# Optimization experiments

Hardware: AMD Instinct MI355X
Metric: run time of the kernel (lower is better)

## Reference

```python
import jax, jax.numpy as jnp
import numpy as np

N_NODES = 50000
N_EDGES = 800000
D_IN = 128
D_HID = 256


def setup_inputs() -> dict:
    key = jax.random.key(0)
    ks = jax.random.split(key, 8)
    x = jax.random.normal(ks[0], (N_NODES, D_IN), dtype=jnp.float32)
    edge_index = jax.random.randint(ks[1], (2, N_EDGES), 0, N_NODES, dtype=jnp.int32)
    s1 = 1.0 / np.sqrt(D_IN)
    s2 = 1.0 / np.sqrt(D_HID)
    W1_l = jax.random.uniform(ks[2], (D_IN, D_HID), jnp.float32, -s1, s1)
    W1_r = jax.random.uniform(ks[3], (D_IN, D_HID), jnp.float32, -s1, s1)
    b1 = jax.random.uniform(ks[4], (D_HID,), jnp.float32, -s1, s1)
    W2_l = jax.random.uniform(ks[5], (D_HID, D_HID), jnp.float32, -s2, s2)
    W2_r = jax.random.uniform(ks[6], (D_HID, D_HID), jnp.float32, -s2, s2)
    b2 = jax.random.uniform(ks[7], (D_HID,), jnp.float32, -s2, s2)
    return {"x": x, "edge_index": edge_index,
            "W1_l": W1_l, "W1_r": W1_r, "b1": b1,
            "W2_l": W2_l, "W2_r": W2_r, "b2": b2}


def _sage_conv(x, src, dst, deg_inv, W_l, W_r, b):
    # mean-aggregate neighbor features at destination nodes, then
    # out = lin_l(mean_neighbors) + lin_r(x)  (PyG SAGEConv, mean aggr)
    msgs = x[src]                                              # [E, d]  irregular gather
    agg = jax.ops.segment_sum(msgs, dst, num_segments=x.shape[0])  # [N, d] scatter-add
    mean = agg * deg_inv[:, None]
    return mean @ W_l + x @ W_r + b


def reference(x, edge_index, W1_l, W1_r, b1, W2_l, W2_r, b2):
    src, dst = edge_index[0], edge_index[1]
    n = x.shape[0]
    deg = jax.ops.segment_sum(jnp.ones_like(dst, dtype=x.dtype), dst, num_segments=n)
    deg_inv = jnp.where(deg > 0, 1.0 / jnp.maximum(deg, 1.0), 0.0)
    h = jax.nn.relu(_sage_conv(x, src, dst, deg_inv, W1_l, W1_r, b1))
    # dropout is identity in eval mode
    out = jax.nn.relu(_sage_conv(h, src, dst, deg_inv, W2_l, W2_r, b2))
    return out
```

## Files before the change

kernel.cpp:

```cpp
#include <hip/hip_runtime.h>
#include <hip/hip_bf16.h>


#define DIN 128
#define DH  256
#define ELLW 64

typedef __attribute__((ext_vector_type(8))) short short8v;
typedef __attribute__((ext_vector_type(4))) float float4v;
typedef __attribute__((ext_vector_type(2))) float float2v;

__device__ __forceinline__ void gload_lds16(const void* g, void* l) {
    __builtin_amdgcn_global_load_lds((const __attribute__((address_space(1))) void*)g,
                                     (__attribute__((address_space(3))) void*)l, 16, 0, 0);
}
__device__ __forceinline__ float bf2f(unsigned short u) {
    union { unsigned int i; float f; } c; c.i = ((unsigned int)u) << 16; return c.f;
}
__device__ __forceinline__ unsigned short f2bf(float f) {
    union { float f; unsigned int i; } c; c.f = f;
    unsigned int lsb = (c.i >> 16) & 1u;
    return (unsigned short)((c.i + 0x7fffu + lsb) >> 16);
}
__device__ __host__ __forceinline__ int permcol(int q) {
    return ((q >> 6) << 6) + ((q & 3) << 4) + ((q >> 2) & 15);
}
__device__ __host__ __forceinline__ int permout(int p) {
    return (((p >> 6) << 4) + (p & 15)) * 4 + ((p >> 4) & 3);
}

__global__ __launch_bounds__(256) void prologue(const float* __restrict__ x,
                                                const float* __restrict__ W1l,
                                                const float* __restrict__ W1r,
                                                const float* __restrict__ W2l,
                                                const float* __restrict__ W2r,
                                                unsigned short* __restrict__ Wt1,
                                                unsigned short* __restrict__ Wt2,
                                                unsigned short* __restrict__ Acat1,
                                                unsigned char* __restrict__ xf8,
                                                const int* __restrict__ src,
                                                const int* __restrict__ dst,
                                                int* __restrict__ cnt,
                                                unsigned short* __restrict__ ell,
                                                int N, int E) {
    const int tid = threadIdx.x;
    const int gtid = blockIdx.x * 256 + tid;
    const int nthr = gridDim.x * 256;

    for (int id = gtid; id < 256 * 256 + 256 * 512; id += nthr) {
        if (id < 256 * 256) {
            int n = id >> 8, k = id & 255;
            float v = (k < 128) ? W1l[k * 256 + n] : W1r[(k - 128) * 256 + n];
            Wt1[n * 256 + k] = f2bf(v);
        } else {
            int id2 = id - 256 * 256;
            int n = id2 >> 9, k = id2 & 511;
            int tc = permout(n);
            float v = (k < 256) ? W2l[permcol(k) * 256 + tc]
                                : W2r[permcol(k - 256) * 256 + tc];
            Wt2[n * 512 + k] = f2bf(v);
        }
    }

    for (int id = gtid; id < N * 32; id += nthr) {
        int base = id * 4;
        float4 v = *(const float4*)(x + base);
        int row = base >> 7, c = base & 127;
        ushort4 o;
        o.x = f2bf(v.x); o.y = f2bf(v.y); o.z = f2bf(v.z); o.w = f2bf(v.w);
        *(ushort4*)(Acat1 + (size_t)row * 256 + 128 + c) = o;
        int p = __builtin_amdgcn_cvt_pk_fp8_f32(v.x, v.y, 0, false);
        p = __builtin_amdgcn_cvt_pk_fp8_f32(v.z, v.w, p, true);
        *(unsigned int*)(xf8 + (size_t)row * 128 + c) = (unsigned int)p;
    }

    int xc = blockIdx.x & 7;
    int bslot = blockIdx.x >> 3;
    int nslot = gridDim.x >> 3;
    int per = (((E + nslot - 1) / nslot) + 7) & ~7;
    int lo = bslot * per;
    int hi = min(lo + per, E);
    for (int base = lo + tid * 8; base + 7 < hi; base += 256 * 8) {
        int4 da = *(const int4*)(dst + base);
        int4 db = *(const int4*)(dst + base + 4);
        int4 sa = *(const int4*)(src + base);
        int4 sb = *(const int4*)(src + base + 4);
        int dd[8] = {da.x, da.y, da.z, da.w, db.x, db.y, db.z, db.w};
        int ss[8] = {sa.x, sa.y, sa.z, sa.w, sb.x, sb.y, sb.z, sb.w};
#pragma unroll
        for (int q = 0; q < 8; ++q) {
            if (((dd[q] >> 6) & 7) == xc) {
                int p = atomicAdd(&cnt[dd[q]], 1);
                if (p < ELLW) ell[(size_t)dd[q] * ELLW + p] = (unsigned short)ss[q];
            }
        }
    }
    int tail = lo + ((hi > lo ? (hi - lo) : 0) & ~7);
    if (tid < (hi - tail)) {
        int e = tail + tid;
        int d = dst[e];
        if (((d >> 6) & 7) == xc) {
            int p = atomicAdd(&cnt[d], 1);
            if (p < ELLW) ell[(size_t)d * ELLW + p] = (unsigned short)src[e];
        }
    }
}

template <int ROWB, int WSTR>
__global__ __launch_bounds__(256) void agg_wpn(const unsigned char* __restrict__ f8,
                                               const unsigned short* __restrict__ ell,
                                               const int* __restrict__ cnt,
                                               unsigned short* __restrict__ outp, int N) {
    constexpr int LANES = ROWB / 4;
    constexpr int NPB = 256 / LANES;
    int tid = threadIdx.x;
    int node = blockIdx.x * NPB + tid / LANES;
    int lane = tid % LANES;
    if (node >= N) return;
    int cn = cnt[node];
    int dg = min(cn, ELLW);
    const unsigned short* row = ell + (size_t)node * ELLW;
    const unsigned char* fb = f8 + (size_t)lane * 4;
    float a0 = 0.f, a1 = 0.f, a2 = 0.f, a3 = 0.f;
    int j = 0;
    for (; j + 8 <= dg; j += 8) {
        short8v i8 = *(const short8v*)(row + j);
        unsigned int v[8];
#pragma unroll
        for (int q = 0; q < 8; ++q)
            v[q] = *(const unsigned int*)(fb + (size_t)(unsigned short)i8[q] * ROWB);
#pragma unroll
        for (int q = 0; q < 8; ++q) {
            float2v lo = __builtin_amdgcn_cvt_pk_f32_fp8((int)v[q], false);
            float2v hi = __builtin_amdgcn_cvt_pk_f32_fp8((int)v[q], true);
            a0 += lo[0]; a1 += lo[1]; a2 += hi[0]; a3 += hi[1];
        }
    }
    for (; j < dg; ++j) {
        unsigned int v = *(const unsigned int*)(fb + (size_t)row[j] * ROWB);
        float2v lo = __builtin_amdgcn_cvt_pk_f32_fp8((int)v, false);
        float2v hi = __builtin_amdgcn_cvt_pk_f32_fp8((int)v, true);
        a0 += lo[0]; a1 += lo[1]; a2 += hi[0]; a3 += hi[1];
    }
    float di = (cn > 0) ? 1.0f / (float)cn : 0.0f;
    ushort4 o;
    o.x = f2bf(a0 * di); o.y = f2bf(a1 * di);
    o.z = f2bf(a2 * di); o.w = f2bf(a3 * di);
    *(ushort4*)(outp + (size_t)node * WSTR + lane * 4) = o;
}

template <int OUT_BF16>
__global__ __launch_bounds__(512) void gemm_mfma(const unsigned short* __restrict__ A, int lda,
                                                 const unsigned short* __restrict__ Wt, int K,
                                                 const float* __restrict__ bias,
                                                 float* __restrict__ outF,
                                                 unsigned short* __restrict__ outB, int ldo,
                                                 unsigned char* __restrict__ outF8,
                                                 int M) {
    __shared__ __align__(16) char lds[49152];
    char* ldsA = lds;
    char* ldsB = lds + 16384;

    const int tid = threadIdx.x;
    const int lane = tid & 63;
    const int wid = tid >> 6;
    const int wm = wid >> 2, wn = wid & 3;
    const int m0 = blockIdx.x * 128;

    float4v acc[4][4];
#pragma unroll
    for (int i = 0; i < 4; ++i)
#pragma unroll
        for (int j = 0; j < 4; ++j) acc[i][j] = (float4v)(0.f);

    int rA[2], cA[2], rB[4], cB[4];
#pragma unroll
    for (int i = 0; i < 2; ++i) {
        int blin = i * 8192 + tid * 16;
        int bdat = blin ^ (((blin >> 7) & 7) << 4);
        rA[i] = min(m0 + (bdat >> 7), M - 1);
        cA[i] = (bdat & 127) >> 1;
    }
#pragma unroll
    for (int i = 0; i < 4; ++i) {
        int blin = i * 8192 + tid * 16;
        int bdat = blin ^ (((blin >> 7) & 7) << 4);
        rB[i] = bdat >> 7;
        cB[i] = (bdat & 127) >> 1;
    }

    for (int kc = 0; kc < K; kc += 64) {
#pragma unroll
        for (int i = 0; i < 2; ++i)
            gload_lds16(A + (size_t)rA[i] * lda + kc + cA[i],
                        ldsA + i * 8192 + wid * 1024);
#pragma unroll
        for (int i = 0; i < 4; ++i)
            gload_lds16(Wt + (size_t)rB[i] * K + kc + cB[i],
                        ldsB + i * 8192 + wid * 1024);
        __syncthreads();

#pragma unroll
        for (int ks = 0; ks < 2; ++ks) {
            short8v af[4], bf[4];
            int cbyte = (ks * 32 + ((lane >> 4) << 3)) * 2;
#pragma unroll
            for (int mi = 0; mi < 4; ++mi) {
                int r = wm * 64 + mi * 16 + (lane & 15);
                int bdat = (r << 7) + cbyte;
                int blin = bdat ^ (((r & 7)) << 4);
                af[mi] = *(const short8v*)(ldsA + blin);
            }
#pragma unroll
            for (int ni = 0; ni < 4; ++ni) {
                int r = wn * 64 + ni * 16 + (lane & 15);
                int bdat = (r << 7) + cbyte;
                int blin = bdat ^ (((r & 7)) << 4);
                bf[ni] = *(const short8v*)(ldsB + blin);
            }
#pragma unroll
            for (int mi = 0; mi < 4; ++mi)
#pragma unroll
                for (int ni = 0; ni < 4; ++ni)
                    acc[mi][ni] = __builtin_amdgcn_mfma_f32_16x16x32_bf16(
                        af[mi], bf[ni], acc[mi][ni], 0, 0, 0);
        }
        __syncthreads();
    }

    const int cl = lane & 15;
    const int rq = (lane >> 4) * 4;
    if (OUT_BF16) {
        const int pbase = (wn * 16 + cl) * 4;
        float bvn[4];
#pragma unroll
        for (int ni = 0; ni < 4; ++ni) bvn[ni] = bias[wn * 64 + ni * 16 + cl];
#pragma unroll
        for (int mi = 0; mi < 4; ++mi) {
#pragma unroll
            for (int j = 0; j < 4; ++j) {
                int gr = m0 + wm * 64 + mi * 16 + rq + j;
                if (gr < M) {
                    float v0 = fmaxf(acc[mi][0][j] + bvn[0], 0.f);
                    float v1 = fmaxf(acc[mi][1][j] + bvn[1], 0.f);
                    float v2 = fmaxf(acc[mi][2][j] + bvn[2], 0.f);
                    float v3 = fmaxf(acc[mi][3][j] + bvn[3], 0.f);
                    ushort4 hb;
                    hb.x = f2bf(v0); hb.y = f2bf(v1);
                    hb.z = f2bf(v2); hb.w = f2bf(v3);
                    *(ushort4*)(outB + (size_t)gr * ldo + pbase) = hb;
                    int pb = __builtin_amdgcn_cvt_pk_fp8_f32(v0, v1, 0, false);
                    pb = __builtin_amdgcn_cvt_pk_fp8_f32(v2, v3, pb, true);
                    *(unsigned int*)(outF8 + (size_t)gr * 256 + pbase) = (unsigned int)pb;
                }
            }
        }
    } else {
        const int obase = (wn * 16 + cl) * 4;
        float4 bv = *(const float4*)(bias + obase);
#pragma unroll
        for (int mi = 0; mi < 4; ++mi) {
#pragma unroll
            for (int j = 0; j < 4; ++j) {
                int gr = m0 + wm * 64 + mi * 16 + rq + j;
                if (gr < M) {
                    float4 o;
                    o.x = fmaxf(acc[mi][0][j] + bv.x, 0.f);
                    o.y = fmaxf(acc[mi][1][j] + bv.y, 0.f);
                    o.z = fmaxf(acc[mi][2][j] + bv.z, 0.f);
                    o.w = fmaxf(acc[mi][3][j] + bv.w, 0.f);
                    *(float4*)(outF + (size_t)gr * 256 + obase) = o;
                }
            }
        }
    }
}

extern "C" void kernel_launch(void* const* d_in, const int* in_sizes, int n_in,
                              void* d_out, int out_size, void* d_ws, size_t ws_size,
                              hipStream_t stream) {
    const float* x   = (const float*)d_in[0];
    const int*   ei  = (const int*)d_in[1];
    const float* W1l = (const float*)d_in[2];
    const float* W1r = (const float*)d_in[3];
    const float* b1  = (const float*)d_in[4];
    const float* W2l = (const float*)d_in[5];
    const float* W2r = (const float*)d_in[6];
    const float* b2  = (const float*)d_in[7];
    float* out = (float*)d_out;

    int N = in_sizes[0] / DIN;
    int E = in_sizes[1] / 2;
    const int* srcI = ei;
    const int* dstI = ei + E;

    char* w = (char*)d_ws;
    auto alloc = [&](size_t bytes) -> char* {
        char* p = w;
        w += (bytes + 255) & ~(size_t)255;
        return p;
    };
    int* cnt = (int*)alloc((size_t)N * 4);
    unsigned short* ell = (unsigned short*)alloc((size_t)N * ELLW * 2);
    unsigned short* Acat1 = (unsigned short*)alloc((size_t)N * 256 * 2);
    unsigned short* Acat2 = (unsigned short*)alloc((size_t)N * 512 * 2);
    unsigned short* Wt1   = (unsigned short*)alloc((size_t)256 * 256 * 2);
    unsigned short* Wt2   = (unsigned short*)alloc((size_t)256 * 512 * 2);
    unsigned char*  hf8   = (unsigned char*)alloc((size_t)N * 256);
    unsigned char*  xf8   = (unsigned char*)Acat2;

    float* b2p = (float*)alloc(256 * 4);

    (void)hipMemsetAsync(cnt, 0, (size_t)N * 4, stream);
    prologue<<<2048, 256, 0, stream>>>(x, W1l, W1r, W2l, W2r, Wt1, Wt2,
                                       Acat1, xf8, srcI, dstI, cnt, ell, N, E);
    (void)b2p;

    int gridM = (N + 127) / 128;

    agg_wpn<128, 256><<<(N + 7) / 8, 256, 0, stream>>>(xf8, ell, cnt, Acat1, N);
    gemm_mfma<1><<<gridM, 512, 0, stream>>>(Acat1, 256, Wt1, 256, b1,
                                            nullptr, Acat2 + 256, 512, hf8, N);
    agg_wpn<256, 512><<<(N + 3) / 4, 256, 0, stream>>>(hf8, ell, cnt, Acat2, N);
    gemm_mfma<0><<<gridM, 512, 0, stream>>>(Acat2, 512, Wt2, 512, b2,
                                            out, nullptr, 256, nullptr, N);
}
```

Before: 154.5 us.

## Split prologue blocks into conversion and ELL-build roles; unroll gather by 16

The prologue grid is now split by role. The first 512 blocks do weight transposition and x conversion, and the remaining 1536 blocks build the ELL adjacency with atomics, so the two phases run concurrently on different blocks instead of one after the other in every block. The aggregation kernel also gains a 16-wide unrolled gather loop that keeps more independent fp8 row loads in flight per lane. The cost is fewer blocks for each phase and higher register pressure in the aggregation kernel. An unused bias buffer allocation is also removed.

Result: faster. 151.5 us (-2.0%).

```diff
diff --git a/kernel.cpp b/kernel.cpp
--- a/kernel.cpp
+++ b/kernel.cpp
@@ -5,6 +5,7 @@
 #define DIN 128
 #define DH  256
 #define ELLW 64
+#define NCONV 512
 
 typedef __attribute__((ext_vector_type(8))) short short8v;
 typedef __attribute__((ext_vector_type(4))) float float4v;
@@ -44,64 +45,67 @@
                                                 unsigned short* __restrict__ ell,
                                                 int N, int E) {
     const int tid = threadIdx.x;
-    const int gtid = blockIdx.x * 256 + tid;
-    const int nthr = gridDim.x * 256;
-
-    for (int id = gtid; id < 256 * 256 + 256 * 512; id += nthr) {
-        if (id < 256 * 256) {
-            int n = id >> 8, k = id & 255;
-            float v = (k < 128) ? W1l[k * 256 + n] : W1r[(k - 128) * 256 + n];
-            Wt1[n * 256 + k] = f2bf(v);
-        } else {
-            int id2 = id - 256 * 256;
-            int n = id2 >> 9, k = id2 & 511;
-            int tc = permout(n);
-            float v = (k < 256) ? W2l[permcol(k) * 256 + tc]
-                                : W2r[permcol(k - 256) * 256 + tc];
-            Wt2[n * 512 + k] = f2bf(v);
-        }
-    }
-
-    for (int id = gtid; id < N * 32; id += nthr) {
-        int base = id * 4;
-        float4 v = *(const float4*)(x + base);
-        int row = base >> 7, c = base & 127;
-        ushort4 o;
-        o.x = f2bf(v.x); o.y = f2bf(v.y); o.z = f2bf(v.z); o.w = f2bf(v.w);
-        *(ushort4*)(Acat1 + (size_t)row * 256 + 128 + c) = o;
-        int p = __builtin_amdgcn_cvt_pk_fp8_f32(v.x, v.y, 0, false);
-        p = __builtin_amdgcn_cvt_pk_fp8_f32(v.z, v.w, p, true);
-        *(unsigned int*)(xf8 + (size_t)row * 128 + c) = (unsigned int)p;
-    }
-
-    int xc = blockIdx.x & 7;
-    int bslot = blockIdx.x >> 3;
-    int nslot = gridDim.x >> 3;
-    int per = (((E + nslot - 1) / nslot) + 7) & ~7;
-    int lo = bslot * per;
-    int hi = min(lo + per, E);
-    for (int base = lo + tid * 8; base + 7 < hi; base += 256 * 8) {
-        int4 da = *(const int4*)(dst + base);
-        int4 db = *(const int4*)(dst + base + 4);
-        int4 sa = *(const int4*)(src + base);
-        int4 sb = *(const int4*)(src + base + 4);
-        int dd[8] = {da.x, da.y, da.z, da.w, db.x, db.y, db.z, db.w};
-        int ss[8] = {sa.x, sa.y, sa.z, sa.w, sb.x, sb.y, sb.z, sb.w};
-#pragma unroll
-        for (int q = 0; q < 8; ++q) {
-            if (((dd[q] >> 6) & 7) == xc) {
-                int p = atomicAdd(&cnt[dd[q]], 1);
-                if (p < ELLW) ell[(size_t)dd[q] * ELLW + p] = (unsigned short)ss[q];
-            }
-        }
-    }
-    int tail = lo + ((hi > lo ? (hi - lo) : 0) & ~7);
-    if (tid < (hi - tail)) {
-        int e = tail + tid;
-        int d = dst[e];
-        if (((d >> 6) & 7) == xc) {
-            int p = atomicAdd(&cnt[d], 1);
-            if (p < ELLW) ell[(size_t)d * ELLW + p] = (unsigned short)src[e];
+
+    if (blockIdx.x < NCONV) {
+        const int gtid = blockIdx.x * 256 + tid;
+        const int nthr = NCONV * 256;
+
+        for (int id = gtid; id < 256 * 256 + 256 * 512; id += nthr) {
+            if (id < 256 * 256) {
+                int n = id >> 8, k = id & 255;
+                float v = (k < 128) ? W1l[k * 256 + n] : W1r[(k - 128) * 256 + n];
+                Wt1[n * 256 + k] = f2bf(v);
+            } else {
+                int id2 = id - 256 * 256;
+                int n = id2 >> 9, k = id2 & 511;
+                int tc = permout(n);
+                float v = (k < 256) ? W2l[permcol(k) * 256 + tc]
+                                    : W2r[permcol(k - 256) * 256 + tc];
+                Wt2[n * 512 + k] = f2bf(v);
+            }
+        }
+        for (int id = gtid; id < N * 32; id += nthr) {
+            int base = id * 4;
+            float4 v = *(const float4*)(x + base);
+            int row = base >> 7, c = base & 127;
+            ushort4 o;
+            o.x = f2bf(v.x); o.y = f2bf(v.y); o.z = f2bf(v.z); o.w = f2bf(v.w);
+            *(ushort4*)(Acat1 + (size_t)row * 256 + 128 + c) = o;
+            int p = __builtin_amdgcn_cvt_pk_fp8_f32(v.x, v.y, 0, false);
+            p = __builtin_amdgcn_cvt_pk_fp8_f32(v.z, v.w, p, true);
+            *(unsigned int*)(xf8 + (size_t)row * 128 + c) = (unsigned int)p;
+        }
+    } else {
+        int idx = blockIdx.x - NCONV;
+        int xc = idx & 7;
+        int bslot = idx >> 3;
+        int nslot = (gridDim.x - NCONV) >> 3;
+        int per = (((E + nslot - 1) / nslot) + 7) & ~7;
+        int lo = bslot * per;
+        int hi = min(lo + per, E);
+        for (int base = lo + tid * 8; base + 7 < hi; base += 256 * 8) {
+            int4 da = *(const int4*)(dst + base);
+            int4 db = *(const int4*)(dst + base + 4);
+            int4 sa = *(const int4*)(src + base);
+            int4 sb = *(const int4*)(src + base + 4);
+            int dd[8] = {da.x, da.y, da.z, da.w, db.x, db.y, db.z, db.w};
+            int ss[8] = {sa.x, sa.y, sa.z, sa.w, sb.x, sb.y, sb.z, sb.w};
+#pragma unroll
+            for (int q = 0; q < 8; ++q) {
+                if (((dd[q] >> 6) & 7) == xc) {
+                    int p = atomicAdd(&cnt[dd[q]], 1);
+                    if (p < ELLW) ell[(size_t)dd[q] * ELLW + p] = (unsigned short)ss[q];
+                }
+            }
+        }
+        int tail = lo + ((hi > lo ? (hi - lo) : 0) & ~7);
+        if (tid < (hi - tail)) {
+            int e = tail + tid;
+            int d = dst[e];
+            if (((d >> 6) & 7) == xc) {
+                int p = atomicAdd(&cnt[d], 1);
+                if (p < ELLW) ell[(size_t)d * ELLW + p] = (unsigned short)src[e];
+            }
         }
     }
 }
@@ -123,6 +127,23 @@
     const unsigned char* fb = f8 + (size_t)lane * 4;
     float a0 = 0.f, a1 = 0.f, a2 = 0.f, a3 = 0.f;
     int j = 0;
+    for (; j + 16 <= dg; j += 16) {
+        short8v i8a = *(const short8v*)(row + j);
+        short8v i8b = *(const short8v*)(row + j + 8);
+        unsigned int v[16];
+#pragma unroll
+        for (int q = 0; q < 8; ++q)
+            v[q] = *(const unsigned int*)(fb + (size_t)(unsigned short)i8a[q] * ROWB);
+#pragma unroll
+        for (int q = 0; q < 8; ++q)
+            v[8 + q] = *(const unsigned int*)(fb + (size_t)(unsigned short)i8b[q] * ROWB);
+#pragma unroll
+        for (int q = 0; q < 16; ++q) {
+            float2v lo = __builtin_amdgcn_cvt_pk_f32_fp8((int)v[q], false);
+            float2v hi = __builtin_amdgcn_cvt_pk_f32_fp8((int)v[q], true);
+            a0 += lo[0]; a1 += lo[1]; a2 += hi[0]; a3 += hi[1];
+        }
+    }
     for (; j + 8 <= dg; j += 8) {
         short8v i8 = *(const short8v*)(row + j);
         unsigned int v[8];
@@ -309,12 +330,9 @@
     unsigned char*  hf8   = (unsigned char*)alloc((size_t)N * 256);
     unsigned char*  xf8   = (unsigned char*)Acat2;
 
-    float* b2p = (float*)alloc(256 * 4);
-
     (void)hipMemsetAsync(cnt, 0, (size_t)N * 4, stream);
     prologue<<<2048, 256, 0, stream>>>(x, W1l, W1r, W2l, W2r, Wt1, Wt2,
                                        Acat1, xf8, srcI, dstI, cnt, ell, N, E);
-    (void)b2p;
 
     int gridM = (N + 127) / 128;
 
```
